# Optimization experiments

Hardware: AMD Instinct MI355X
Metric: run time of the kernel (lower is better)

Reference implementation:

```python
import jax, jax.numpy as jnp
import numpy as np

B, C_IN, T, N, C_OUT = 4, 32, 8, 2000, 64
E = 16000
H1, H2 = 128, 256


def _glorot(key, fan_in, fan_out):
    scale = jnp.sqrt(2.0 / (fan_in + fan_out)).astype(jnp.float32)
    return jax.random.normal(key, (fan_in, fan_out), jnp.float32) * scale


def setup_inputs() -> dict:
    key = jax.random.key(0)
    ks = jax.random.split(key, 8)
    x = jax.random.normal(ks[0], (B, C_IN, T, N), jnp.float32)
    edge_index = jax.random.randint(ks[1], (2, E), 0, N, dtype=jnp.int64)
    edge_weight = jax.random.uniform(ks[2], (E,), jnp.float32)
    W1 = _glorot(ks[3], C_IN, H1); b1 = jnp.zeros((H1,), jnp.float32)
    W2 = _glorot(ks[4], H1, H2);   b2 = jnp.zeros((H2,), jnp.float32)
    W3 = _glorot(ks[5], H2, C_OUT); b3 = jnp.zeros((C_OUT,), jnp.float32)
    return {"x": x, "edge_index": edge_index, "edge_weight": edge_weight,
            "W1": W1, "b1": b1, "W2": W2, "b2": b2, "W3": W3, "b3": b3}


def reference(x, edge_index, edge_weight, W1, b1, W2, b2, W3, b3):
    # x: [B, C_in, T, N] -> node-major [B, T, N, C_in]
    h = jnp.transpose(x, (0, 2, 3, 1))
    n = x.shape[-1]
    src, dst = edge_index[0], edge_index[1]
    # GCNConv default: add self-loops with weight 1, symmetric normalization
    loops = jnp.arange(n)
    src_f = jnp.concatenate([src, loops])
    dst_f = jnp.concatenate([dst, loops])
    ew_f = jnp.concatenate([edge_weight, jnp.ones((n,), x.dtype)])
    deg = jnp.zeros((n,), x.dtype).at[dst_f].add(ew_f)  # deg >= 1 via self-loops
    dinv = jax.lax.rsqrt(deg)
    norm = dinv[src_f] * ew_f * dinv[dst_f]  # [E+N]

    def gcn(h, W, b):
        h = h @ W                                      # [B,T,N,C']
        msg = h[:, :, src_f, :] * norm[None, None, :, None]  # [B,T,E+N,C']
        agg = jnp.zeros_like(h).at[:, :, dst_f, :].add(msg)
        return agg + b

    # original: conv1 -> dropout -> conv2 -> dropout -> conv3 -> relu
    # (dropout is identity in eval mode; no activation between convs)
    h = gcn(h, W1, b1)
    h = gcn(h, W2, b2)
    h = jax.nn.relu(gcn(h, W3, b3))
    # stack/transpose in original yields [B, C_out, T, N]
    return jnp.transpose(h, (0, 3, 1, 2))
```

## Files before the change

### kernel.cpp

```cpp
#include <hip/hip_runtime.h>
#include <hip/hip_bf16.h>

#define NB 4
#define CIN 32
#define TT 8
#define NN 2000
#define NE 16000
#define H1C 128
#define H2C 256
#define COUT 64
#define BT (NB*TT)
#define BNN 2048
#define WINV (1.0f/65535.0f)

__global__ __launch_bounds__(1024) void k_sss(
    const float* __restrict__ x,
    const int* __restrict__ src, const int* __restrict__ dst,
    const float* __restrict__ ew,
    const float* __restrict__ W1, const float* __restrict__ b1,
    const float* __restrict__ W2, const float* __restrict__ b2,
    const float* __restrict__ W3,
    float* __restrict__ r1f, float* __restrict__ r2f,
    float* __restrict__ W123_g, float* __restrict__ d1_g, float* __restrict__ d2_g,
    float* __restrict__ C3)
{
    __shared__ unsigned int cmp[NE];
    __shared__ float4 Y[BNN];
    __shared__ float  idg[BNN];
    __shared__ unsigned int rp[BNN + 1];
    __shared__ int cc_[BNN];
    __shared__ int ssc[256];

    const int tid = threadIdx.x;
    const int cg = blockIdx.x, bt = blockIdx.y;
    const int b = bt >> 3, t = bt & 7;

    if (bt == 1) {
        float* W3s  = (float*)cmp;
        float* W23s = (float*)cmp + H2C * 8;
        const int j0 = cg * 8;

        for (int i = tid; i < H2C * 8; i += 1024)
            W3s[i] = W3[(size_t)(i >> 3) * COUT + j0 + (i & 7)];
        __syncthreads();

        for (int r = tid >> 3; r < H1C + 1; r += 128) {
            int j = tid & 7;
            const float* wrow = (r < H1C) ? (W2 + (size_t)r * H2C) : b2;
            float a0 = 0, a1 = 0, a2 = 0, a3 = 0;
            for (int k = 0; k < H2C; k += 4) {
                float4 wv = *(const float4*)(wrow + k);
                a0 += wv.x * W3s[(k + 0) * 8 + j];
                a1 += wv.y * W3s[(k + 1) * 8 + j];
                a2 += wv.z * W3s[(k + 2) * 8 + j];
                a3 += wv.w * W3s[(k + 3) * 8 + j];
            }
            W23s[r * 8 + j] = (a0 + a1) + (a2 + a3);
        }
        __syncthreads();

        for (int r = tid >> 3; r < CIN + 1; r += 128) {
            int j = tid & 7;
            const float* wrow = (r < CIN) ? (W1 + (size_t)r * H1C) : b1;
            float a0 = 0, a1 = 0, a2 = 0, a3 = 0;
            for (int k = 0; k < H1C; k += 4) {
                float4 wv = *(const float4*)(wrow + k);
                a0 += wv.x * W23s[(k + 0) * 8 + j];
                a1 += wv.y * W23s[(k + 1) * 8 + j];
                a2 += wv.z * W23s[(k + 2) * 8 + j];
                a3 += wv.w * W23s[(k + 3) * 8 + j];
            }
            float acc = (a0 + a1) + (a2 + a3);
            if (r < CIN) W123_g[(size_t)r * COUT + j0 + j] = acc;
            else         d1_g[j0 + j] = acc;
        }
        if (tid < 8) d2_g[j0 + tid] = W23s[H1C * 8 + tid];
        __syncthreads();
    }

    for (int i = tid; i < BNN; i += 1024) cc_[i] = 0;
    __syncthreads();
    #pragma unroll
    for (int i = 0; i < 16; i++) {
        int e = tid + i * 1024;
        if (e < NE) atomicAdd(&cc_[dst[e]], 1);
    }
    __syncthreads();

    int local[8];
    if (tid < 256) {
        int base = tid * 8, sum = 0;
        #pragma unroll
        for (int i = 0; i < 8; i++) {
            int v = cc_[base + i];
            local[i] = sum;
            sum += v;
        }
        ssc[tid] = sum;
    }
    __syncthreads();
    for (int off = 1; off < 256; off <<= 1) {
        int v = 0;
        if (tid < 256 && tid >= off) v = ssc[tid - off];
        __syncthreads();
        if (tid < 256 && tid >= off) ssc[tid] += v;
        __syncthreads();
    }
    if (tid < 256) {
        int ce = (tid > 0) ? ssc[tid - 1] : 0;
        int base = tid * 8;
        #pragma unroll
        for (int i = 0; i < 8; i++) {
            int v = ce + local[i];
            rp[base + i] = v;
            cc_[base + i] = v;
        }
        if (tid == 255) rp[BNN] = ssc[255];
    }
    __syncthreads();

    #pragma unroll
    for (int i = 0; i < 16; i++) {
        int e = tid + i * 1024;
        if (e < NE) {
            int d = dst[e];
            unsigned int w16 = __float2uint_rn(ew[e] * 65535.0f);
            if (w16 > 65535u) w16 = 65535u;
            int pos = atomicAdd(&cc_[d], 1);
            cmp[pos] = ((unsigned int)src[e] << 16) | w16;
        }
    }
    __syncthreads();

    for (int n = tid; n < BNN; n += 1024) {
        float s = 0.f;
        for (unsigned int p = rp[n]; p < rp[n + 1]; p++)
            s += (float)(cmp[p] & 0xffffu);
        idg[n] = 1.0f / (1.0f + s * WINV);
    }
    __syncthreads();

    if (cg == 0 && bt == 0) {
        float* Ys = (float*)Y;
        for (int n = tid; n < BNN; n += 1024) Ys[n] = sqrtf(idg[n]);
        __syncthreads();
        for (int n = tid; n < NN; n += 1024) {
            float s = 0.f;
            for (unsigned int p = rp[n]; p < rp[n + 1]; p++) {
                unsigned int g = cmp[p];
                s += (float)(g & 0xffffu) * Ys[g >> 16];
            }
            float r = Ys[n] * (Ys[n] + s * WINV);
            r1f[n] = r;
            Ys[BNN + n] = Ys[n] * r;
        }
        __syncthreads();
        for (int n = tid; n < NN; n += 1024) {
            float s = 0.f;
            for (unsigned int p = rp[n]; p < rp[n + 1]; p++) {
                unsigned int g = cmp[p];
                s += (float)(g & 0xffffu) * Ys[BNN + (g >> 16)];
            }
            r2f[n] = Ys[n] * (Ys[BNN + n] + s * WINV);
        }
        __syncthreads();
    }

    for (int n = tid; n < NN; n += 1024) {
        float sq = sqrtf(idg[n]);
        float4 v;
        v.x = x[(((size_t)b * CIN + cg * 4 + 0) * TT + t) * NN + n] * sq;
        v.y = x[(((size_t)b * CIN + cg * 4 + 1) * TT + t) * NN + n] * sq;
        v.z = x[(((size_t)b * CIN + cg * 4 + 2) * TT + t) * NN + n] * sq;
        v.w = x[(((size_t)b * CIN + cg * 4 + 3) * TT + t) * NN + n] * sq;
        Y[n] = v;
    }
    __syncthreads();

    const int n0 = tid, n1 = tid + 1024;
    const unsigned int rp0 = rp[n0], re0 = rp[n0 + 1];
    const unsigned int rp1 = rp[n1], re1 = rp[n1 + 1];
    const int cn0 = (int)(re0 - rp0), cn1 = (int)(re1 - rp1);
    const int mx = max(cn0, cn1);

    for (int pass = 0; pass < 3; pass++) {
        float4 a0 = Y[n0];
        float4 a1 = Y[n1];
        float sx0 = 0, sy0 = 0, sz0 = 0, sw0 = 0;
        float sx1 = 0, sy1 = 0, sz1 = 0, sw1 = 0;
        for (int k = 0; k < mx; k++) {
            if (k < cn0) {
                unsigned int g = cmp[rp0 + k];
                float w = (float)(g & 0xffffu);
                float4 y = Y[g >> 16];
                sx0 += w * y.x; sy0 += w * y.y; sz0 += w * y.z; sw0 += w * y.w;
            }
            if (k < cn1) {
                unsigned int g = cmp[rp1 + k];
                float w = (float)(g & 0xffffu);
                float4 y = Y[g >> 16];
                sx1 += w * y.x; sy1 += w * y.y; sz1 += w * y.z; sw1 += w * y.w;
            }
        }
        a0.x += sx0 * WINV; a0.y += sy0 * WINV; a0.z += sz0 * WINV; a0.w += sw0 * WINV;
        a1.x += sx1 * WINV; a1.y += sy1 * WINV; a1.z += sz1 * WINV; a1.w += sw1 * WINV;

        if (pass < 2) {
            __syncthreads();
            float g0 = idg[n0];
            Y[n0] = make_float4(a0.x * g0, a0.y * g0, a0.z * g0, a0.w * g0);
            float g1 = idg[n1];
            Y[n1] = make_float4(a1.x * g1, a1.y * g1, a1.z * g1, a1.w * g1);
            __syncthreads();
        } else {
            float s0 = sqrtf(idg[n0]);
            float* base = C3 + ((size_t)bt * CIN + cg * 4) * NN;
            base[0 * NN + n0] = a0.x * s0;
            base[1 * NN + n0] = a0.y * s0;
            base[2 * NN + n0] = a0.z * s0;
            base[3 * NN + n0] = a0.w * s0;
            if (n1 < NN) {
                float s1 = sqrtf(idg[n1]);
                base[0 * NN + n1] = a1.x * s1;
                base[1 * NN + n1] = a1.y * s1;
                base[2 * NN + n1] = a1.z * s1;
                base[3 * NN + n1] = a1.w * s1;
            }
        }
    }
}

__global__ __launch_bounds__(256) void k_out(
    const float* __restrict__ C3,
    const float* __restrict__ W123,
    const float* __restrict__ d1, const float* __restrict__ d2,
    const float* __restrict__ b3,
    const float* __restrict__ r1f, const float* __restrict__ r2f,
    float* __restrict__ out)
{
    __shared__ float Cs[CIN][65];
    __shared__ float Ws[CIN][64];
    __shared__ float Os[64][65];
    __shared__ float d1s[64], d2s[64], b3s[64], r1s[64], r2s[64];
    const int tid = threadIdx.x;
    const int bt = blockIdx.y, b = bt >> 3, t = bt & 7;
    const int n0 = blockIdx.x * 64;

    for (int i = tid; i < CIN * 64; i += 256) {
        int ch = i >> 6, nn = i & 63;
        int n = n0 + nn;
        Cs[ch][nn] = (n < NN) ? C3[((size_t)bt * CIN + ch) * NN + n] : 0.f;
    }
    for (int i = tid; i < CIN * 64; i += 256)
        Ws[i >> 6][i & 63] = W123[i];
    if (tid < 64) {
        d1s[tid] = d1[tid];
        d2s[tid] = d2[tid];
        b3s[tid] = b3[tid];
        int n = n0 + tid;
        r1s[tid] = (n < NN) ? r1f[n] : 0.f;
        r2s[tid] = (n < NN) ? r2f[n] : 0.f;
    }
    __syncthreads();

    const int c = tid & 63, g = tid >> 6;
    for (int i = 0; i < 16; i++) {
        int nn = g * 16 + i;
        float acc = r2s[nn] * d1s[c] + r1s[nn] * d2s[c] + b3s[c];
        #pragma unroll
        for (int k = 0; k < CIN; k++) acc += Cs[k][nn] * Ws[k][c];
        Os[nn][c] = fmaxf(acc, 0.f);
    }
    __syncthreads();

    #pragma unroll
    for (int pass = 0; pass < 16; pass++) {
        int cc = g + pass * 4;
        int n = n0 + (tid & 63);
        if (n < NN)
            out[(((size_t)b * COUT + cc) * TT + t) * NN + n] = Os[tid & 63][cc];
    }
}


extern "C" void kernel_launch(void* const* d_in, const int* in_sizes, int n_in,
                              void* d_out, int out_size, void* d_ws, size_t ws_size,
                              hipStream_t stream) {
    (void)in_sizes; (void)n_in; (void)out_size; (void)ws_size;

    const float* x  = (const float*)d_in[0];
    const int*   ei = (const int*)d_in[1];
    const float* ew = (const float*)d_in[2];
    const float* W1 = (const float*)d_in[3];
    const float* b1 = (const float*)d_in[4];
    const float* W2 = (const float*)d_in[5];
    const float* b2 = (const float*)d_in[6];
    const float* W3 = (const float*)d_in[7];
    const float* b3 = (const float*)d_in[8];
    float* out = (float*)d_out;

    const int* src = ei;
    const int* dst = ei + NE;

    float* wsf  = (float*)d_ws;
    float* r1f  = wsf;
    float* r2f  = wsf + 2048;
    float* W123 = wsf + 4096;
    float* d1   = wsf + 6144;
    float* d2   = wsf + 6208;
    float* C3   = wsf + 6272;

    k_sss<<<dim3(8, BT), dim3(1024), 0, stream>>>(
        x, src, dst, ew, W1, b1, W2, b2, W3,
        r1f, r2f, W123, d1, d2, C3);

    k_out<<<dim3(32, BT), dim3(256), 0, stream>>>(
        C3, W123, d1, d2, b3, r1f, r2f, out);
}
```

Measured before the change: 59.47 us.

## Pad CSR rows to four, sort nodes by degree, use planar SoA features

Edge loads are vectorised as int4/float4. Each CSR row is padded to a multiple of four and the padding slots are zeroed, so the aggregation loop can read uint4 edge groups. Nodes are bucketed by degree through a shared histogram and prefix sum, so the two nodes a thread handles have similar degree, which cuts warp divergence in the imbalanced gather. Features move from float4 AoS to planar SoA in shared memory, and the final store reads from shared memory. This costs an extra binning pass, more shared memory for the padded CSR, and 16-bit row pointers.

Result: slower. 70.15 us (+18.0%).

```diff
diff --git a/kernel.cpp b/kernel.cpp
--- a/kernel.cpp
+++ b/kernel.cpp
@@ -11,6 +11,7 @@
 #define COUT 64
 #define BT (NB*TT)
 #define BNN 2048
+#define CMPSZ 22016
 #define WINV (1.0f/65535.0f)
 
 __global__ __launch_bounds__(1024) void k_sss(
@@ -24,10 +25,10 @@
     float* __restrict__ W123_g, float* __restrict__ d1_g, float* __restrict__ d2_g,
     float* __restrict__ C3)
 {
-    __shared__ unsigned int cmp[NE];
-    __shared__ float4 Y[BNN];
-    __shared__ float  idg[BNN];
-    __shared__ unsigned int rp[BNN + 1];
+    __shared__ unsigned int cmp[CMPSZ];
+    __shared__ float Yp[4 * BNN];
+    __shared__ float idg[BNN];
+    __shared__ unsigned short rp[BNN + 2];
     __shared__ int cc_[BNN];
     __shared__ int ssc[256];
 
@@ -80,10 +81,19 @@
 
     for (int i = tid; i < BNN; i += 1024) cc_[i] = 0;
     __syncthreads();
-    #pragma unroll
-    for (int i = 0; i < 16; i++) {
-        int e = tid + i * 1024;
-        if (e < NE) atomicAdd(&cc_[dst[e]], 1);
+    const int4*   dst4 = (const int4*)dst;
+    const int4*   src4 = (const int4*)src;
+    const float4* ew4  = (const float4*)ew;
+    #pragma unroll
+    for (int i = 0; i < 4; i++) {
+        int j = tid + i * 1024;
+        if (j < NE / 4) {
+            int4 d4 = dst4[j];
+            atomicAdd(&cc_[d4.x], 1);
+            atomicAdd(&cc_[d4.y], 1);
+            atomicAdd(&cc_[d4.z], 1);
+            atomicAdd(&cc_[d4.w], 1);
+        }
     }
     __syncthreads();
 
@@ -92,9 +102,9 @@
         int base = tid * 8, sum = 0;
         #pragma unroll
         for (int i = 0; i < 8; i++) {
-            int v = cc_[base + i];
+            int cnp = (cc_[base + i] + 3) & ~3;
             local[i] = sum;
-            sum += v;
+            sum += cnp;
         }
         ssc[tid] = sum;
     }
@@ -112,121 +122,183 @@
         #pragma unroll
         for (int i = 0; i < 8; i++) {
             int v = ce + local[i];
-            rp[base + i] = v;
+            rp[base + i] = (unsigned short)v;
             cc_[base + i] = v;
         }
-        if (tid == 255) rp[BNN] = ssc[255];
-    }
-    __syncthreads();
-
-    #pragma unroll
-    for (int i = 0; i < 16; i++) {
-        int e = tid + i * 1024;
-        if (e < NE) {
-            int d = dst[e];
-            unsigned int w16 = __float2uint_rn(ew[e] * 65535.0f);
-            if (w16 > 65535u) w16 = 65535u;
-            int pos = atomicAdd(&cc_[d], 1);
-            cmp[pos] = ((unsigned int)src[e] << 16) | w16;
-        }
-    }
-    __syncthreads();
-
-    for (int n = tid; n < BNN; n += 1024) {
+        if (tid == 255) rp[BNN] = (unsigned short)ssc[255];
+    }
+    __syncthreads();
+
+    #pragma unroll
+    for (int i = 0; i < 4; i++) {
+        int j = tid + i * 1024;
+        if (j < NE / 4) {
+            int4 s4 = src4[j]; int4 d4 = dst4[j]; float4 w4 = ew4[j];
+            unsigned int w; int pos;
+            w = __float2uint_rn(w4.x * 65535.0f); if (w > 65535u) w = 65535u;
+            pos = atomicAdd(&cc_[d4.x], 1); cmp[pos] = ((unsigned)s4.x << 16) | w;
+            w = __float2uint_rn(w4.y * 65535.0f); if (w > 65535u) w = 65535u;
+            pos = atomicAdd(&cc_[d4.y], 1); cmp[pos] = ((unsigned)s4.y << 16) | w;
+            w = __float2uint_rn(w4.z * 65535.0f); if (w > 65535u) w = 65535u;
+            pos = atomicAdd(&cc_[d4.z], 1); cmp[pos] = ((unsigned)s4.z << 16) | w;
+            w = __float2uint_rn(w4.w * 65535.0f); if (w > 65535u) w = 65535u;
+            pos = atomicAdd(&cc_[d4.w], 1); cmp[pos] = ((unsigned)s4.w << 16) | w;
+        }
+    }
+    __syncthreads();
+
+    #pragma unroll
+    for (int h = 0; h < 2; h++) {
+        int n = tid + h * 1024;
+        int p0 = rp[n], p1 = cc_[n], pe = rp[n + 1];
         float s = 0.f;
-        for (unsigned int p = rp[n]; p < rp[n + 1]; p++)
-            s += (float)(cmp[p] & 0xffffu);
+        for (int p = p0; p < p1; p++) s += (float)(cmp[p] & 0xffffu);
+        for (int p = p1; p < pe; p++) cmp[p] = 0u;
         idg[n] = 1.0f / (1.0f + s * WINV);
     }
     __syncthreads();
 
+    if (tid < 128) ssc[tid] = 0;
+    __syncthreads();
+    #pragma unroll
+    for (int h = 0; h < 2; h++) {
+        int n = tid + h * 1024;
+        int bin = min((int)(rp[n + 1] - rp[n]) >> 2, 63);
+        atomicAdd(&ssc[bin], 1);
+    }
+    __syncthreads();
+    if (tid < 64) {
+        int v = ssc[tid], s = v;
+        #pragma unroll
+        for (int off = 1; off < 64; off <<= 1) {
+            int u = __shfl_up(s, off);
+            if (tid >= off) s += u;
+        }
+        ssc[64 + tid] = s - v;
+    }
+    __syncthreads();
+    #pragma unroll
+    for (int h = 0; h < 2; h++) {
+        int n = tid + h * 1024;
+        int bin = min((int)(rp[n + 1] - rp[n]) >> 2, 63);
+        int pos = atomicAdd(&ssc[64 + bin], 1);
+        cc_[pos] = n;
+    }
+    __syncthreads();
+
     if (cg == 0 && bt == 0) {
-        float* Ys = (float*)Y;
-        for (int n = tid; n < BNN; n += 1024) Ys[n] = sqrtf(idg[n]);
+        for (int n = tid; n < BNN; n += 1024) Yp[n] = sqrtf(idg[n]);
         __syncthreads();
         for (int n = tid; n < NN; n += 1024) {
             float s = 0.f;
-            for (unsigned int p = rp[n]; p < rp[n + 1]; p++) {
-                unsigned int g = cmp[p];
-                s += (float)(g & 0xffffu) * Ys[g >> 16];
-            }
-            float r = Ys[n] * (Ys[n] + s * WINV);
+            for (int p = rp[n]; p < rp[n + 1]; p++) {
+                unsigned g = cmp[p];
+                s += (float)(g & 0xffffu) * Yp[g >> 16];
+            }
+            float r = Yp[n] * (Yp[n] + s * WINV);
             r1f[n] = r;
-            Ys[BNN + n] = Ys[n] * r;
+            Yp[BNN + n] = Yp[n] * r;
         }
         __syncthreads();
         for (int n = tid; n < NN; n += 1024) {
             float s = 0.f;
-            for (unsigned int p = rp[n]; p < rp[n + 1]; p++) {
-                unsigned int g = cmp[p];
-                s += (float)(g & 0xffffu) * Ys[BNN + (g >> 16)];
-            }
-            r2f[n] = Ys[n] * (Ys[BNN + n] + s * WINV);
-        }
-        __syncthreads();
-    }
-
+            for (int p = rp[n]; p < rp[n + 1]; p++) {
+                unsigned g = cmp[p];
+                s += (float)(g & 0xffffu) * Yp[BNN + (g >> 16)];
+            }
+            r2f[n] = Yp[n] * (Yp[BNN + n] + s * WINV);
+        }
+        __syncthreads();
+    }
+
+    for (int n = tid; n < BNN; n += 1024) {
+        if (n < NN) {
+            float sq = sqrtf(idg[n]);
+            Yp[0 * BNN + n] = x[(((size_t)b * CIN + cg * 4 + 0) * TT + t) * NN + n] * sq;
+            Yp[1 * BNN + n] = x[(((size_t)b * CIN + cg * 4 + 1) * TT + t) * NN + n] * sq;
+            Yp[2 * BNN + n] = x[(((size_t)b * CIN + cg * 4 + 2) * TT + t) * NN + n] * sq;
+            Yp[3 * BNN + n] = x[(((size_t)b * CIN + cg * 4 + 3) * TT + t) * NN + n] * sq;
+        } else {
+            Yp[0 * BNN + n] = 0.f; Yp[1 * BNN + n] = 0.f;
+            Yp[2 * BNN + n] = 0.f; Yp[3 * BNN + n] = 0.f;
+        }
+    }
+    __syncthreads();
+
+    const int na = cc_[2 * tid], nb = cc_[2 * tid + 1];
+    const int ra = rp[na]; const int ca = (int)rp[na + 1] - ra;
+    const int rb = rp[nb]; const int cb = (int)rp[nb + 1] - rb;
+    const int mx = max(ca, cb);
+
+    for (int pass = 0; pass < 3; pass++) {
+        float a0 = Yp[0 * BNN + na], a1 = Yp[1 * BNN + na];
+        float a2 = Yp[2 * BNN + na], a3 = Yp[3 * BNN + na];
+        float c0 = Yp[0 * BNN + nb], c1 = Yp[1 * BNN + nb];
+        float c2 = Yp[2 * BNN + nb], c3 = Yp[3 * BNN + nb];
+        for (int k = 0; k < mx; k += 4) {
+            if (k < ca) {
+                uint4 e = *(const uint4*)&cmp[ra + k];
+                {
+                    float w = (float)(e.x & 0xffffu) * WINV; int s = e.x >> 16;
+                    a0 += w * Yp[s]; a1 += w * Yp[BNN + s];
+                    a2 += w * Yp[2 * BNN + s]; a3 += w * Yp[3 * BNN + s];
+                }
+                {
+                    float w = (float)(e.y & 0xffffu) * WINV; int s = e.y >> 16;
+                    a0 += w * Yp[s]; a1 += w * Yp[BNN + s];
+                    a2 += w * Yp[2 * BNN + s]; a3 += w * Yp[3 * BNN + s];
+                }
+                {
+                    float w = (float)(e.z & 0xffffu) * WINV; int s = e.z >> 16;
+                    a0 += w * Yp[s]; a1 += w * Yp[BNN + s];
+                    a2 += w * Yp[2 * BNN + s]; a3 += w * Yp[3 * BNN + s];
+                }
+                {
+                    float w = (float)(e.w & 0xffffu) * WINV; int s = e.w >> 16;
+                    a0 += w * Yp[s]; a1 += w * Yp[BNN + s];
+                    a2 += w * Yp[2 * BNN + s]; a3 += w * Yp[3 * BNN + s];
+                }
+            }
+            if (k < cb) {
+                uint4 e = *(const uint4*)&cmp[rb + k];
+                {
+                    float w = (float)(e.x & 0xffffu) * WINV; int s = e.x >> 16;
+                    c0 += w * Yp[s]; c1 += w * Yp[BNN + s];
+                    c2 += w * Yp[2 * BNN + s]; c3 += w * Yp[3 * BNN + s];
+                }
+                {
+                    float w = (float)(e.y & 0xffffu) * WINV; int s = e.y >> 16;
+                    c0 += w * Yp[s]; c1 += w * Yp[BNN + s];
+                    c2 += w * Yp[2 * BNN + s]; c3 += w * Yp[3 * BNN + s];
+                }
+                {
+                    float w = (float)(e.z & 0xffffu) * WINV; int s = e.z >> 16;
+                    c0 += w * Yp[s]; c1 += w * Yp[BNN + s];
+                    c2 += w * Yp[2 * BNN + s]; c3 += w * Yp[3 * BNN + s];
+                }
+                {
+                    float w = (float)(e.w & 0xffffu) * WINV; int s = e.w >> 16;
+                    c0 += w * Yp[s]; c1 += w * Yp[BNN + s];
+                    c2 += w * Yp[2 * BNN + s]; c3 += w * Yp[3 * BNN + s];
+                }
+            }
+        }
+        __syncthreads();
+        float sa = (pass < 2) ? idg[na] : sqrtf(idg[na]);
+        float sb = (pass < 2) ? idg[nb] : sqrtf(idg[nb]);
+        Yp[0 * BNN + na] = a0 * sa; Yp[1 * BNN + na] = a1 * sa;
+        Yp[2 * BNN + na] = a2 * sa; Yp[3 * BNN + na] = a3 * sa;
+        Yp[0 * BNN + nb] = c0 * sb; Yp[1 * BNN + nb] = c1 * sb;
+        Yp[2 * BNN + nb] = c2 * sb; Yp[3 * BNN + nb] = c3 * sb;
+        __syncthreads();
+    }
+
+    float* base = C3 + ((size_t)bt * CIN + cg * 4) * NN;
     for (int n = tid; n < NN; n += 1024) {
-        float sq = sqrtf(idg[n]);
-        float4 v;
-        v.x = x[(((size_t)b * CIN + cg * 4 + 0) * TT + t) * NN + n] * sq;
-        v.y = x[(((size_t)b * CIN + cg * 4 + 1) * TT + t) * NN + n] * sq;
-        v.z = x[(((size_t)b * CIN + cg * 4 + 2) * TT + t) * NN + n] * sq;
-        v.w = x[(((size_t)b * CIN + cg * 4 + 3) * TT + t) * NN + n] * sq;
-        Y[n] = v;
-    }
-    __syncthreads();
-
-    const int n0 = tid, n1 = tid + 1024;
-    const unsigned int rp0 = rp[n0], re0 = rp[n0 + 1];
-    const unsigned int rp1 = rp[n1], re1 = rp[n1 + 1];
-    const int cn0 = (int)(re0 - rp0), cn1 = (int)(re1 - rp1);
-    const int mx = max(cn0, cn1);
-
-    for (int pass = 0; pass < 3; pass++) {
-        float4 a0 = Y[n0];
-        float4 a1 = Y[n1];
-        float sx0 = 0, sy0 = 0, sz0 = 0, sw0 = 0;
-        float sx1 = 0, sy1 = 0, sz1 = 0, sw1 = 0;
-        for (int k = 0; k < mx; k++) {
-            if (k < cn0) {
-                unsigned int g = cmp[rp0 + k];
-                float w = (float)(g & 0xffffu);
-                float4 y = Y[g >> 16];
-                sx0 += w * y.x; sy0 += w * y.y; sz0 += w * y.z; sw0 += w * y.w;
-            }
-            if (k < cn1) {
-                unsigned int g = cmp[rp1 + k];
-                float w = (float)(g & 0xffffu);
-                float4 y = Y[g >> 16];
-                sx1 += w * y.x; sy1 += w * y.y; sz1 += w * y.z; sw1 += w * y.w;
-            }
-        }
-        a0.x += sx0 * WINV; a0.y += sy0 * WINV; a0.z += sz0 * WINV; a0.w += sw0 * WINV;
-        a1.x += sx1 * WINV; a1.y += sy1 * WINV; a1.z += sz1 * WINV; a1.w += sw1 * WINV;
-
-        if (pass < 2) {
-            __syncthreads();
-            float g0 = idg[n0];
-            Y[n0] = make_float4(a0.x * g0, a0.y * g0, a0.z * g0, a0.w * g0);
-            float g1 = idg[n1];
-            Y[n1] = make_float4(a1.x * g1, a1.y * g1, a1.z * g1, a1.w * g1);
-            __syncthreads();
-        } else {
-            float s0 = sqrtf(idg[n0]);
-            float* base = C3 + ((size_t)bt * CIN + cg * 4) * NN;
-            base[0 * NN + n0] = a0.x * s0;
-            base[1 * NN + n0] = a0.y * s0;
-            base[2 * NN + n0] = a0.z * s0;
-            base[3 * NN + n0] = a0.w * s0;
-            if (n1 < NN) {
-                float s1 = sqrtf(idg[n1]);
-                base[0 * NN + n1] = a1.x * s1;
-                base[1 * NN + n1] = a1.y * s1;
-                base[2 * NN + n1] = a1.z * s1;
-                base[3 * NN + n1] = a1.w * s1;
-            }
-        }
+        base[0 * NN + n] = Yp[0 * BNN + n];
+        base[1 * NN + n] = Yp[1 * BNN + n];
+        base[2 * NN + n] = Yp[2 * BNN + n];
+        base[3 * NN + n] = Yp[3 * BNN + n];
     }
 }
 
```

## Fuse output projection kernel into main kernel via cooperative grid sync

Applied to the files above, without the earlier changes.

Merges the second kernel, which does the 32→64 projection, bias and ReLU, into the first kernel. A cooperative-groups grid-wide sync separates the two phases, and the fused kernel is launched with hipLaunchCooperativeKernel. The aim is to remove the second launch and its gap. Each 1024-thread block now handles four 64-node output tiles, reusing the shared-memory space of the first phase. The risks are the cost of the grid barrier, lower parallelism in the output phase (256 blocks instead of 1024), and the requirement that all 256 blocks be co-resident.

After: 102.9 us. +73.0%, slower.

```diff
diff --git a/kernel.cpp b/kernel.cpp
--- a/kernel.cpp
+++ b/kernel.cpp
@@ -1,5 +1,6 @@
 #include <hip/hip_runtime.h>
 #include <hip/hip_bf16.h>
+#include <hip/hip_cooperative_groups.h>
 
 #define NB 4
 #define CIN 32
@@ -13,16 +14,17 @@
 #define BNN 2048
 #define WINV (1.0f/65535.0f)
 
-__global__ __launch_bounds__(1024) void k_sss(
+__global__ __launch_bounds__(1024) void k_fused(
     const float* __restrict__ x,
     const int* __restrict__ src, const int* __restrict__ dst,
     const float* __restrict__ ew,
     const float* __restrict__ W1, const float* __restrict__ b1,
     const float* __restrict__ W2, const float* __restrict__ b2,
-    const float* __restrict__ W3,
+    const float* __restrict__ W3, const float* __restrict__ b3,
     float* __restrict__ r1f, float* __restrict__ r2f,
     float* __restrict__ W123_g, float* __restrict__ d1_g, float* __restrict__ d2_g,
-    float* __restrict__ C3)
+    float* __restrict__ C3,
+    float* __restrict__ out)
 {
     __shared__ unsigned int cmp[NE];
     __shared__ float4 Y[BNN];
@@ -228,57 +230,61 @@
             }
         }
     }
-}
-
-__global__ __launch_bounds__(256) void k_out(
-    const float* __restrict__ C3,
-    const float* __restrict__ W123,
-    const float* __restrict__ d1, const float* __restrict__ d2,
-    const float* __restrict__ b3,
-    const float* __restrict__ r1f, const float* __restrict__ r2f,
-    float* __restrict__ out)
-{
-    __shared__ float Cs[CIN][65];
-    __shared__ float Ws[CIN][64];
-    __shared__ float Os[64][65];
-    __shared__ float d1s[64], d2s[64], b3s[64], r1s[64], r2s[64];
-    const int tid = threadIdx.x;
-    const int bt = blockIdx.y, b = bt >> 3, t = bt & 7;
-    const int n0 = blockIdx.x * 64;
-
-    for (int i = tid; i < CIN * 64; i += 256) {
-        int ch = i >> 6, nn = i & 63;
-        int n = n0 + nn;
-        Cs[ch][nn] = (n < NN) ? C3[((size_t)bt * CIN + ch) * NN + n] : 0.f;
-    }
-    for (int i = tid; i < CIN * 64; i += 256)
-        Ws[i >> 6][i & 63] = W123[i];
+
+    cooperative_groups::this_grid().sync();
+
+    float* Wsl = (float*)cmp;
+    float* Csl = (float*)cmp + 2048;
+    float* Osl = (float*)cmp + 4096;
+    float* d1s = (float*)cmp + 8256;
+    float* d2s = d1s + 64;
+    float* b3s = d2s + 64;
+    float* r1s = b3s + 64;
+    float* r2s = r1s + 64;
+
+    for (int i = tid; i < 2048; i += 1024) Wsl[i] = W123_g[i];
     if (tid < 64) {
-        d1s[tid] = d1[tid];
-        d2s[tid] = d2[tid];
+        d1s[tid] = d1_g[tid];
+        d2s[tid] = d2_g[tid];
         b3s[tid] = b3[tid];
-        int n = n0 + tid;
-        r1s[tid] = (n < NN) ? r1f[n] : 0.f;
-        r2s[tid] = (n < NN) ? r2f[n] : 0.f;
     }
     __syncthreads();
 
     const int c = tid & 63, g = tid >> 6;
-    for (int i = 0; i < 16; i++) {
-        int nn = g * 16 + i;
-        float acc = r2s[nn] * d1s[c] + r1s[nn] * d2s[c] + b3s[c];
+    #pragma unroll
+    for (int q = 0; q < 4; q++) {
+        const int nt0 = (cg * 4 + q) * 64;
+        for (int i = tid; i < CIN * 64; i += 1024) {
+            int ch = i >> 6, nn = i & 63;
+            int n = nt0 + nn;
+            Csl[ch * 64 + nn] = (n < NN) ? C3[((size_t)bt * CIN + ch) * NN + n] : 0.f;
+        }
+        if (tid < 64) {
+            int n = nt0 + tid;
+            r1s[tid] = (n < NN) ? r1f[n] : 0.f;
+            r2s[tid] = (n < NN) ? r2f[n] : 0.f;
+        }
+        __syncthreads();
+
         #pragma unroll
-        for (int k = 0; k < CIN; k++) acc += Cs[k][nn] * Ws[k][c];
-        Os[nn][c] = fmaxf(acc, 0.f);
-    }
-    __syncthreads();
-
-    #pragma unroll
-    for (int pass = 0; pass < 16; pass++) {
-        int cc = g + pass * 4;
-        int n = n0 + (tid & 63);
-        if (n < NN)
-            out[(((size_t)b * COUT + cc) * TT + t) * NN + n] = Os[tid & 63][cc];
+        for (int i = 0; i < 4; i++) {
+            int nn = g * 4 + i;
+            float acc = r2s[nn] * d1s[c] + r1s[nn] * d2s[c] + b3s[c];
+            #pragma unroll
+            for (int k = 0; k < CIN; k++)
+                acc += Csl[k * 64 + nn] * Wsl[k * 64 + c];
+            Osl[nn * 65 + c] = fmaxf(acc, 0.f);
+        }
+        __syncthreads();
+
+        #pragma unroll
+        for (int pass = 0; pass < 4; pass++) {
+            int cc = g + pass * 16;
+            int n = nt0 + c;
+            if (n < NN)
+                out[(((size_t)b * COUT + cc) * TT + t) * NN + n] = Osl[c * 65 + cc];
+        }
+        __syncthreads();
     }
 }
 
@@ -310,10 +316,12 @@
     float* d2   = wsf + 6208;
     float* C3   = wsf + 6272;
 
-    k_sss<<<dim3(8, BT), dim3(1024), 0, stream>>>(
-        x, src, dst, ew, W1, b1, W2, b2, W3,
-        r1f, r2f, W123, d1, d2, C3);
-
-    k_out<<<dim3(32, BT), dim3(256), 0, stream>>>(
-        C3, W123, d1, d2, b3, r1f, r2f, out);
+    void* args[] = {
+        (void*)&x, (void*)&src, (void*)&dst, (void*)&ew,
+        (void*)&W1, (void*)&b1, (void*)&W2, (void*)&b2, (void*)&W3, (void*)&b3,
+        (void*)&r1f, (void*)&r2f, (void*)&W123, (void*)&d1, (void*)&d2,
+        (void*)&C3, (void*)&out
+    };
+    hipLaunchCooperativeKernel((void*)k_fused, dim3(8, BT), dim3(1024),
+                               args, 0, stream);
 }
```

## Sort nodes by in-degree to balance per-thread gather work across wavefronts

Applied to the files above, without the earlier changes.

Adds a counting sort of nodes by in-degree, built from a shared-memory histogram, a wave prefix scan and a scatter, so each thread handles two nodes of similar degree and neighbouring lanes in a wavefront have similar loop trip counts. This is meant to cut divergence in the sparse aggregation loop, where the max-degree bound was previously set by arbitrary node pairs. Because the assignment is now permuted, the final pass writes back into shared Y and a separate coalesced loop stores C3. This adds sort overhead and one extra sync per block, and neighbouring lanes now store to scattered Y locations.

Result: slower. 64.10 us (+7.8%).

```diff
diff --git a/kernel.cpp b/kernel.cpp
--- a/kernel.cpp
+++ b/kernel.cpp
@@ -140,6 +140,34 @@
     }
     __syncthreads();
 
+    if (tid < 128) ssc[tid] = 0;
+    __syncthreads();
+    #pragma unroll
+    for (int h = 0; h < 2; h++) {
+        int n = tid + h * 1024;
+        int bin = min((int)(rp[n + 1] - rp[n]), 63);
+        atomicAdd(&ssc[bin], 1);
+    }
+    __syncthreads();
+    if (tid < 64) {
+        int v = ssc[tid], s = v;
+        #pragma unroll
+        for (int off = 1; off < 64; off <<= 1) {
+            int u = __shfl_up(s, off);
+            if (tid >= off) s += u;
+        }
+        ssc[64 + tid] = s - v;
+    }
+    __syncthreads();
+    #pragma unroll
+    for (int h = 0; h < 2; h++) {
+        int n = tid + h * 1024;
+        int bin = min((int)(rp[n + 1] - rp[n]), 63);
+        int pos = atomicAdd(&ssc[64 + bin], 1);
+        cc_[pos] = n;
+    }
+    __syncthreads();
+
     if (cg == 0 && bt == 0) {
         float* Ys = (float*)Y;
         for (int n = tid; n < BNN; n += 1024) Ys[n] = sqrtf(idg[n]);
@@ -166,26 +194,30 @@
         __syncthreads();
     }
 
-    for (int n = tid; n < NN; n += 1024) {
-        float sq = sqrtf(idg[n]);
-        float4 v;
-        v.x = x[(((size_t)b * CIN + cg * 4 + 0) * TT + t) * NN + n] * sq;
-        v.y = x[(((size_t)b * CIN + cg * 4 + 1) * TT + t) * NN + n] * sq;
-        v.z = x[(((size_t)b * CIN + cg * 4 + 2) * TT + t) * NN + n] * sq;
-        v.w = x[(((size_t)b * CIN + cg * 4 + 3) * TT + t) * NN + n] * sq;
-        Y[n] = v;
-    }
-    __syncthreads();
-
-    const int n0 = tid, n1 = tid + 1024;
-    const unsigned int rp0 = rp[n0], re0 = rp[n0 + 1];
-    const unsigned int rp1 = rp[n1], re1 = rp[n1 + 1];
+    for (int n = tid; n < BNN; n += 1024) {
+        if (n < NN) {
+            float sq = sqrtf(idg[n]);
+            float4 v;
+            v.x = x[(((size_t)b * CIN + cg * 4 + 0) * TT + t) * NN + n] * sq;
+            v.y = x[(((size_t)b * CIN + cg * 4 + 1) * TT + t) * NN + n] * sq;
+            v.z = x[(((size_t)b * CIN + cg * 4 + 2) * TT + t) * NN + n] * sq;
+            v.w = x[(((size_t)b * CIN + cg * 4 + 3) * TT + t) * NN + n] * sq;
+            Y[n] = v;
+        } else {
+            Y[n] = make_float4(0.f, 0.f, 0.f, 0.f);
+        }
+    }
+    __syncthreads();
+
+    const int na = cc_[2 * tid], nb = cc_[2 * tid + 1];
+    const unsigned int rp0 = rp[na], re0 = rp[na + 1];
+    const unsigned int rp1 = rp[nb], re1 = rp[nb + 1];
     const int cn0 = (int)(re0 - rp0), cn1 = (int)(re1 - rp1);
     const int mx = max(cn0, cn1);
 
     for (int pass = 0; pass < 3; pass++) {
-        float4 a0 = Y[n0];
-        float4 a1 = Y[n1];
+        float4 a0 = Y[na];
+        float4 a1 = Y[nb];
         float sx0 = 0, sy0 = 0, sz0 = 0, sw0 = 0;
         float sx1 = 0, sy1 = 0, sz1 = 0, sw1 = 0;
         for (int k = 0; k < mx; k++) {
@@ -205,28 +237,21 @@
         a0.x += sx0 * WINV; a0.y += sy0 * WINV; a0.z += sz0 * WINV; a0.w += sw0 * WINV;
         a1.x += sx1 * WINV; a1.y += sy1 * WINV; a1.z += sz1 * WINV; a1.w += sw1 * WINV;
 
-        if (pass < 2) {
-            __syncthreads();
-            float g0 = idg[n0];
-            Y[n0] = make_float4(a0.x * g0, a0.y * g0, a0.z * g0, a0.w * g0);
-            float g1 = idg[n1];
-            Y[n1] = make_float4(a1.x * g1, a1.y * g1, a1.z * g1, a1.w * g1);
-            __syncthreads();
-        } else {
-            float s0 = sqrtf(idg[n0]);
-            float* base = C3 + ((size_t)bt * CIN + cg * 4) * NN;
-            base[0 * NN + n0] = a0.x * s0;
-            base[1 * NN + n0] = a0.y * s0;
-            base[2 * NN + n0] = a0.z * s0;
-            base[3 * NN + n0] = a0.w * s0;
-            if (n1 < NN) {
-                float s1 = sqrtf(idg[n1]);
-                base[0 * NN + n1] = a1.x * s1;
-                base[1 * NN + n1] = a1.y * s1;
-                base[2 * NN + n1] = a1.z * s1;
-                base[3 * NN + n1] = a1.w * s1;
-            }
-        }
+        __syncthreads();
+        float sa = (pass < 2) ? idg[na] : sqrtf(idg[na]);
+        float sb = (pass < 2) ? idg[nb] : sqrtf(idg[nb]);
+        Y[na] = make_float4(a0.x * sa, a0.y * sa, a0.z * sa, a0.w * sa);
+        Y[nb] = make_float4(a1.x * sb, a1.y * sb, a1.z * sb, a1.w * sb);
+        __syncthreads();
+    }
+
+    float* base = C3 + ((size_t)bt * CIN + cg * 4) * NN;
+    for (int n = tid; n < NN; n += 1024) {
+        float4 v = Y[n];
+        base[0 * NN + n] = v.x;
+        base[1 * NN + n] = v.y;
+        base[2 * NN + n] = v.z;
+        base[3 * NN + n] = v.w;
     }
 }
 
```
